# Kernel optimization log

Measured on AMD Instinct MI355X. Metric: run time of the kernel, lower is better.

Reference implementation:

```python
import jax, jax.numpy as jnp
import numpy as np
from functools import partial

L, B, D, V = 256, 64, 1024, 32000
N_LAYERS = 2  # wargs.enc_layer_cnt


def _ran_scan(x_seq, c0, Wix, Wic, Wfx, Wfc, Wcx, bi, bf, bc, reverse):
    """RAN over time. x_seq: [L,B,D], c0: [B,D]. Returns (h_seq [L,B,D], c_last).

    Cell: cand = x@Wcx + bc; i = sigma(x@Wix + c@Wic + bi); f = sigma(x@Wfx + c@Wfc + bf)
          c' = i*cand + f*c; h = tanh(c') + x  (residual=True)
    """
    # precompute input projections for all steps (hoisted out of the recurrence)
    xi = x_seq @ Wix + bi   # [L,B,D]
    xf = x_seq @ Wfx + bf
    xc = x_seq @ Wcx + bc

    def step(c, inputs):
        x, xi_t, xf_t, xc_t = inputs
        i = jax.nn.sigmoid(xi_t + c @ Wic)
        f = jax.nn.sigmoid(xf_t + c @ Wfc)
        c_new = i * xc_t + f * c
        h = jnp.tanh(c_new) + x
        return c_new, h

    c_last, hs = jax.lax.scan(step, c0, (x_seq, xi, xf, xc), reverse=reverse)
    return hs, c_last


def setup_inputs() -> dict:
    key = jax.random.key(0)
    ks = jax.random.split(key, 20)
    s = 1.0 / np.sqrt(D)
    xs = jax.random.randint(ks[0], (L, B), 0, V, dtype=jnp.int64)
    emb = jax.random.normal(ks[1], (V, D), dtype=jnp.float32) * s
    emb = emb.at[0].set(0.0)  # padding_idx=PAD(=0)
    def w(k):
        return jax.random.normal(k, (D, D), dtype=jnp.float32) * s
    inp = {"xs": xs, "emb": emb}
    for pfx, off in (("fw", 2), ("bw", 10)):
        inp[pfx + "_Wix"] = w(ks[off + 0])
        inp[pfx + "_Wic"] = w(ks[off + 1])
        inp[pfx + "_Wfx"] = w(ks[off + 2])
        inp[pfx + "_Wfc"] = w(ks[off + 3])
        inp[pfx + "_Wcx"] = w(ks[off + 4])
        inp[pfx + "_bi"] = jnp.zeros((D,), jnp.float32)
        inp[pfx + "_bf"] = jnp.zeros((D,), jnp.float32)
        inp[pfx + "_bc"] = jnp.zeros((D,), jnp.float32)
    return inp


def reference(xs, emb,
              fw_Wix, fw_Wic, fw_Wfx, fw_Wfc, fw_Wcx, fw_bi, fw_bf, fw_bc,
              bw_Wix, bw_Wic, bw_Wfx, bw_Wfc, bw_Wcx, bw_bi, bw_bf, bw_bc):
    x = emb[xs]                         # [L,B,D] token embeddings
    c = jnp.zeros((xs.shape[1], D), dtype=emb.dtype)  # c0 = zeros(B, output_size)
    for _ in range(N_LAYERS):
        # snaker: forward-direction RAN, state c threads into backward pass
        first, c = _ran_scan(x, c, fw_Wix, fw_Wic, fw_Wfx, fw_Wfc, fw_Wcx,
                             fw_bi, fw_bf, fw_bc, reverse=False)
        x, c = _ran_scan(first, c, bw_Wix, bw_Wic, bw_Wfx, bw_Wfc, bw_Wcx,
                         bw_bi, bw_bf, bw_bc, reverse=True)
    return x
```

## Files before the change

### kernel.cpp

```cpp
#include <hip/hip_runtime.h>
#include <hip/hip_bf16.h>

typedef unsigned int u32;
typedef unsigned short u16;
typedef unsigned long long u64;
typedef __attribute__((ext_vector_type(8))) short short8;
typedef __attribute__((ext_vector_type(4))) float floatx4;

#define L_SEQ 256
#define BATCH 64
#define DIM 1024
#define GROUPS 8
#define GWGS 32
#define GROWS 8

__device__ __forceinline__ float b2f(u16 u) {
  union { u32 i; float f; } v; v.i = ((u32)u) << 16; return v.f;
}
__device__ __forceinline__ u16 f2b(float f) {
  union { float f; u32 i; } v; v.f = f;
  u32 r = v.i + 0x7FFFu + ((v.i >> 16) & 1u);
  return (u16)(r >> 16);
}

__device__ __forceinline__ void st_b16_sc(const u16* p, u16 v) {
  asm volatile("global_store_short %0, %1, off sc0 sc1"
               :: "v"((u64)(uintptr_t)p), "v"((u32)v) : "memory");
}

__global__ void zero_cnt(u32* p) {
  #pragma unroll
  for (int i = 0; i < 4; ++i) p[threadIdx.x * 4 + i] = 0;
}

__global__ __launch_bounds__(256) void transpose6(
    const float* __restrict__ w0, const float* __restrict__ w1,
    const float* __restrict__ w2, const float* __restrict__ w3,
    const float* __restrict__ w4, const float* __restrict__ w5,
    u16* __restrict__ wt)
{
  __shared__ u16 tile[64][66];
  const int z = blockIdx.z;
  const float* src = z==0?w0: z==1?w1: z==2?w2: z==3?w3: z==4?w4: w5;
  u16* dst = wt + (size_t)z * DIM * DIM;
  const int k0 = blockIdx.x * 64, n0 = blockIdx.y * 64;
  const int r = threadIdx.x & 63, q = threadIdx.x >> 6;
  #pragma unroll 4
  for (int rep = 0; rep < 16; ++rep) {
    int k = q * 16 + rep;
    tile[k][r] = f2b(src[(size_t)(k0 + k) * DIM + n0 + r]);
  }
  __syncthreads();
  #pragma unroll 4
  for (int rep = 0; rep < 16; ++rep) {
    int n = q * 16 + rep;
    dst[(size_t)(n0 + n) * DIM + k0 + r] = tile[r][n];
  }
}

__global__ __launch_bounds__(256) void embed_gather(
    const int* __restrict__ xs, const float* __restrict__ emb, u16* __restrict__ Xb)
{
  const int t = blockIdx.x * 256 + threadIdx.x;
  const int row = t >> 8, ch = t & 255;
  const int tok = xs[row];
  float4 v = *(const float4*)(emb + (size_t)tok * DIM + ch * 4);
  union { ushort4 s; u16 u[4]; } o;
  o.u[0] = f2b(v.x); o.u[1] = f2b(v.y); o.u[2] = f2b(v.z); o.u[3] = f2b(v.w);
  *(ushort4*)(Xb + (size_t)row * DIM + ch * 4) = o.s;
}

__global__ __launch_bounds__(256) void proj3(
    const u16* __restrict__ X, const u16* __restrict__ WTbase,
    const float* __restrict__ bi, const float* __restrict__ bfp,
    const float* __restrict__ bc,
    u16* __restrict__ XI, u16* __restrict__ XF, u16* __restrict__ XC)
{
  __shared__ __align__(16) u16 ldsA[8 * 64 * 8];
  __shared__ __align__(16) u16 ldsB[8 * 64 * 8];
  const int z = blockIdx.z;
  const u16* WT = WTbase + (size_t)z * DIM * DIM;
  const float* bias = z == 0 ? bi : (z == 1 ? bfp : bc);
  u16* Y = z == 0 ? XI : (z == 1 ? XF : XC);
  const int m0 = blockIdx.x * 128, n0 = blockIdx.y * 128;
  const int tid = threadIdx.x;
  const int l = tid & 63, w = tid >> 6;
  const int wm = w >> 1, wn = w & 1;

  floatx4 acc[4][4];
  #pragma unroll
  for (int i = 0; i < 4; ++i)
    #pragma unroll
    for (int j = 0; j < 4; ++j) acc[i][j] = (floatx4){0, 0, 0, 0};

  const int srow = tid >> 2, sch = tid & 3;
  for (int k0 = 0; k0 < DIM; k0 += 32) {
    #pragma unroll
    for (int rr = 0; rr < 2; ++rr) {
      int row = rr * 64 + srow;
      uint4 va = *(const uint4*)(X  + (size_t)(m0 + row) * DIM + k0 + sch * 8);
      uint4 vb = *(const uint4*)(WT + (size_t)(n0 + row) * DIM + k0 + sch * 8);
      int slot = ((row >> 4) * 64 + (row & 15) + 16 * sch) * 8;
      *(uint4*)(ldsA + slot) = va;
      *(uint4*)(ldsB + slot) = vb;
    }
    __syncthreads();
    short8 af[4], bf8[4];
    #pragma unroll
    for (int i = 0; i < 4; ++i) af[i]  = *(const short8*)(ldsA + ((wm * 4 + i) * 64 + l) * 8);
    #pragma unroll
    for (int j = 0; j < 4; ++j) bf8[j] = *(const short8*)(ldsB + ((wn * 4 + j) * 64 + l) * 8);
    #pragma unroll
    for (int i = 0; i < 4; ++i)
      #pragma unroll
      for (int j = 0; j < 4; ++j)
        acc[i][j] = __builtin_amdgcn_mfma_f32_16x16x32_bf16(af[i], bf8[j], acc[i][j], 0, 0, 0);
    __syncthreads();
  }
  const int lq = l >> 4, lc = l & 15;
  #pragma unroll
  for (int j = 0; j < 4; ++j) {
    int col = n0 + wn * 64 + j * 16 + lc;
    float bv = bias[col];
    #pragma unroll
    for (int i = 0; i < 4; ++i)
      #pragma unroll
      for (int r = 0; r < 4; ++r) {
        int row = m0 + wm * 64 + i * 16 + lq * 4 + r;
        Y[(size_t)row * DIM + col] = f2b(acc[i][j][r] + bv);
      }
  }
}

__device__ __forceinline__ void g_arrive(u32* c) {
  __syncthreads();
  if (threadIdx.x == 0)
    __hip_atomic_fetch_add(c, 1u, __ATOMIC_RELAXED, __HIP_MEMORY_SCOPE_AGENT);
}
__device__ __forceinline__ void g_wait(u32* c, u32 tgt) {
  if (threadIdx.x == 0)
    while (__hip_atomic_load(c, __ATOMIC_RELAXED, __HIP_MEMORY_SCOPE_AGENT) < tgt)
      __builtin_amdgcn_s_sleep(1);
  __syncthreads();
}

__global__ __launch_bounds__(256, 1) void ran_scan_g(
    const float* __restrict__ Wic, const float* __restrict__ Wfc,
    const u16* __restrict__ XI, const u16* __restrict__ XF,
    const u16* __restrict__ XC,
    u16* __restrict__ Xb,
    float* __restrict__ HoutF,
    u16* __restrict__ cbf,
    float* __restrict__ cf32,
    u32* __restrict__ cnt,
    int reverse, int load_c, int write_out)
{
  __shared__ floatx4 part[4][2][2][64];
  const int tid = threadIdx.x, l = tid & 63, w = tid >> 6;
  const int group = blockIdx.x & 7, member = blockIdx.x >> 3;
  const int q = l >> 4, lr = l & 15;
  const int d0 = member * 32;
  const int g8 = group * GROWS;
  u16* cgrp = cbf + (size_t)group * (2 * GROWS * DIM);
  u32* gcnt = cnt + group * 32;
  const int act = (w == 0) && (q < 2);
  const int mrow = q * 4;

  short8 bregs[8][2][2];
  for (int kk8 = 0; kk8 < 8; ++kk8) {
    const int kbase = w * 256 + kk8 * 32 + q * 8;
    #pragma unroll
    for (int nt = 0; nt < 2; ++nt) {
      const int n = d0 + nt * 16 + lr;
      #pragma unroll
      for (int g = 0; g < 2; ++g) {
        const float* W = g ? Wfc : Wic;
        union { short8 v; u16 u[8]; } tmp;
        #pragma unroll
        for (int j = 0; j < 8; ++j) tmp.u[j] = f2b(W[(size_t)(kbase + j) * DIM + n]);
        bregs[kk8][nt][g] = tmp.v;
      }
    }
  }

  float creg[2][4];
  float xi[2][4], xf[2][4], xc[2][4], xv[2][4];
  int t = reverse ? (L_SEQ - 1) : 0;
  const int dt = reverse ? -1 : 1;

  if (act) {
    #pragma unroll
    for (int nt = 0; nt < 2; ++nt)
      #pragma unroll
      for (int r = 0; r < 4; ++r) {
        const int b = g8 + mrow + r, d = d0 + nt * 16 + lr;
        creg[nt][r] = load_c ? cf32[(size_t)b * DIM + d] : 0.0f;
        st_b16_sc(cgrp + (mrow + r) * DIM + d, f2b(creg[nt][r]));
      }
    const size_t base = (size_t)t * (BATCH * DIM);
    #pragma unroll
    for (int nt = 0; nt < 2; ++nt)
      #pragma unroll
      for (int r = 0; r < 4; ++r) {
        const size_t idx = base + (size_t)(g8 + mrow + r) * DIM + d0 + nt * 16 + lr;
        xi[nt][r] = b2f(XI[idx]); xf[nt][r] = b2f(XF[idx]);
        xc[nt][r] = b2f(XC[idx]); xv[nt][r] = b2f(Xb[idx]);
      }
  }

  u32 epoch = 1;
  g_arrive(gcnt);
  g_wait(gcnt, GWGS * epoch); ++epoch;

  for (int step = 0; step < L_SEQ; ++step, t += dt) {
    const size_t base = (size_t)t * (BATCH * DIM);
    const u16* crd = cgrp + (size_t)(step & 1) * (GROWS * DIM);
    u16* cwr = cgrp + (size_t)((step + 1) & 1) * (GROWS * DIM);

    uint4 afr[8];
    if (lr < 8) {
      const u64 ab = (u64)(uintptr_t)crd + (u32)(lr * 2048 + w * 512 + q * 16);
      asm volatile(
        "global_load_dwordx4 %0, %8, off sc0 sc1\n\t"
        "global_load_dwordx4 %1, %8, off offset:64 sc0 sc1\n\t"
        "global_load_dwordx4 %2, %8, off offset:128 sc0 sc1\n\t"
        "global_load_dwordx4 %3, %8, off offset:192 sc0 sc1\n\t"
        "global_load_dwordx4 %4, %8, off offset:256 sc0 sc1\n\t"
        "global_load_dwordx4 %5, %8, off offset:320 sc0 sc1\n\t"
        "global_load_dwordx4 %6, %8, off offset:384 sc0 sc1\n\t"
        "global_load_dwordx4 %7, %8, off offset:448 sc0 sc1\n\t"
        "s_waitcnt vmcnt(0)"
        : "=&v"(afr[0]), "=&v"(afr[1]), "=&v"(afr[2]), "=&v"(afr[3]),
          "=&v"(afr[4]), "=&v"(afr[5]), "=&v"(afr[6]), "=&v"(afr[7])
        : "v"(ab)
        : "memory");
    } else {
      #pragma unroll
      for (int i = 0; i < 8; ++i) afr[i] = (uint4){0, 0, 0, 0};
    }

    floatx4 acc[2][2];
    #pragma unroll
    for (int nt = 0; nt < 2; ++nt)
      #pragma unroll
      for (int g = 0; g < 2; ++g) acc[nt][g] = (floatx4){0, 0, 0, 0};
    #pragma unroll
    for (int kk8 = 0; kk8 < 8; ++kk8) {
      const short8 a = __builtin_bit_cast(short8, afr[kk8]);
      #pragma unroll
      for (int nt = 0; nt < 2; ++nt) {
        acc[nt][0] = __builtin_amdgcn_mfma_f32_16x16x32_bf16(a, bregs[kk8][nt][0], acc[nt][0], 0, 0, 0);
        acc[nt][1] = __builtin_amdgcn_mfma_f32_16x16x32_bf16(a, bregs[kk8][nt][1], acc[nt][1], 0, 0, 0);
      }
    }
    #pragma unroll
    for (int nt = 0; nt < 2; ++nt) {
      part[w][nt][0][l] = acc[nt][0];
      part[w][nt][1][l] = acc[nt][1];
    }
    __syncthreads();

    if (act) {
      floatx4 sI[2], sF[2];
      #pragma unroll
      for (int nt = 0; nt < 2; ++nt) {
        sI[nt] = part[0][nt][0][l]; sF[nt] = part[0][nt][1][l];
        #pragma unroll
        for (int pw = 1; pw < 4; ++pw) { sI[nt] += part[pw][nt][0][l]; sF[nt] += part[pw][nt][1][l]; }
      }
      #pragma unroll
      for (int nt = 0; nt < 2; ++nt)
        #pragma unroll
        for (int r = 0; r < 4; ++r) {
          const float iv = 1.0f / (1.0f + __expf(-(xi[nt][r] + sI[nt][r])));
          const float fv = 1.0f / (1.0f + __expf(-(xf[nt][r] + sF[nt][r])));
          const float cn = iv * xc[nt][r] + fv * creg[nt][r];
          creg[nt][r] = cn;
          const float hv = tanhf(cn) + xv[nt][r];
          const int d = d0 + nt * 16 + lr;
          const size_t idx = base + (size_t)(g8 + mrow + r) * DIM + d;
          __builtin_nontemporal_store(f2b(hv), Xb + idx);
          if (write_out) __builtin_nontemporal_store(hv, HoutF + idx);
          st_b16_sc(cwr + (mrow + r) * DIM + d, f2b(cn));
        }
    }
    g_arrive(gcnt);
    if (act && step + 1 < L_SEQ) {
      const size_t nb = (size_t)(t + dt) * (BATCH * DIM);
      #pragma unroll
      for (int nt = 0; nt < 2; ++nt)
        #pragma unroll
        for (int r = 0; r < 4; ++r) {
          const size_t idx = nb + (size_t)(g8 + mrow + r) * DIM + d0 + nt * 16 + lr;
          xi[nt][r] = b2f(XI[idx]); xf[nt][r] = b2f(XF[idx]);
          xc[nt][r] = b2f(XC[idx]); xv[nt][r] = b2f(Xb[idx]);
        }
    }
    g_wait(gcnt, GWGS * epoch); ++epoch;
  }

  if (act) {
    #pragma unroll
    for (int nt = 0; nt < 2; ++nt)
      #pragma unroll
      for (int r = 0; r < 4; ++r)
        cf32[(size_t)(g8 + mrow + r) * DIM + d0 + nt * 16 + lr] = creg[nt][r];
  }
}

extern "C" void kernel_launch(void* const* d_in, const int* in_sizes, int n_in,
                              void* d_out, int out_size, void* d_ws, size_t ws_size,
                              hipStream_t stream) {
  (void)in_sizes; (void)out_size; (void)ws_size;
  const int* xs = (const int*)d_in[0];
  const float* emb = (const float*)d_in[1];
  const float* W[18];
  for (int i = 0; i < 18 && i < n_in; ++i) W[i] = (const float*)d_in[i];

  char* ws = (char*)d_ws;
  u32* cnt    = (u32*)ws;
  u16* WT     = (u16*)(ws + 8192);
  u16* Xb     = (u16*)(ws + 12591104ull);
  u16* XIb    = (u16*)(ws + 46145536ull);
  u16* XFb    = (u16*)(ws + 79699968ull);
  u16* XCb    = (u16*)(ws + 113254400ull);
  u16* cbf    = (u16*)(ws + 146808832ull);
  float* cf32 = (float*)(ws + 147070976ull);

  zero_cnt<<<1, 256, 0, stream>>>(cnt);
  transpose6<<<dim3(16, 16, 6), 256, 0, stream>>>(W[2], W[4], W[6], W[10], W[12], W[14], WT);
  embed_gather<<<16384, 256, 0, stream>>>(xs, emb, Xb);

  for (int s = 0; s < 4; ++s) {
    const int p = s & 1;
    const u16* WTs = WT + (size_t)p * 3 * DIM * DIM;
    proj3<<<dim3(128, 8, 3), 256, 0, stream>>>(
        Xb, WTs, W[p ? 15 : 7], W[p ? 16 : 8], W[p ? 17 : 9], XIb, XFb, XCb);
    ran_scan_g<<<256, 256, 0, stream>>>(
        W[p ? 11 : 3], W[p ? 13 : 5], XIb, XFb, XCb, Xb, (float*)d_out,
        cbf, cf32, cnt + s * 256, p, s > 0 ? 1 : 0, s == 3 ? 1 : 0);
  }
}
```

Before: 4.701 ms.

## Use XCD-local atomic barrier and packed c-state publish in scan kernel

At startup each workgroup records its XCC id, and the kernel checks whether all 32 members of a group share one XCD. If they do, it takes a path that publishes the c state with non-coherent atomic swaps and polls the counter with atomics without sc1, avoiding device-wide cache coherence traffic. The c state is now written as packed dword stores in a permuted layout, and the weight k-index is remapped to match. The tanh and h output are moved after the publish, and input loads become nontemporal. The change adds a detection barrier, a bounded spin loop, and relies on the hardware placing each group on one XCD.

```diff
diff --git a/kernel.cpp b/kernel.cpp
--- a/kernel.cpp
+++ b/kernel.cpp
@@ -23,14 +23,87 @@
   return (u16)(r >> 16);
 }
 
-__device__ __forceinline__ void st_b16_sc(const u16* p, u16 v) {
-  asm volatile("global_store_short %0, %1, off sc0 sc1"
-               :: "v"((u64)(uintptr_t)p), "v"((u32)v) : "memory");
+__device__ __forceinline__ void st_u32_llc(u32* p, u32 v) {
+  asm volatile("global_store_dword %0, %1, off sc0 sc1"
+               :: "v"((u64)(uintptr_t)p), "v"(v) : "memory");
+}
+__device__ __forceinline__ u32 ld_u32_llc(const u32* p) {
+  u32 v;
+  asm volatile("global_load_dword %0, %1, off sc0 sc1\n\ts_waitcnt vmcnt(0)"
+               : "=v"(v) : "v"((u64)(uintptr_t)p) : "memory");
+  return v;
+}
+
+template<bool LOCAL>
+__device__ __forceinline__ void c_write_publish(
+    u32* gcnt, u16* cwr, int act, int cb_off,
+    u32 pk0, u32 pk1, u32 pk2, u32 pk3)
+{
+  if (act) {
+    const u64 a0 = (u64)(uintptr_t)cwr + (u32)cb_off;
+    const u64 a1 = a0 + 2048, a2 = a0 + 4096, a3 = a0 + 6144;
+    if constexpr (LOCAL) {
+      u32 o0, o1, o2, o3;
+      asm volatile(
+        "global_atomic_swap %0, %4, %8, off sc0\n\t"
+        "global_atomic_swap %1, %5, %9, off sc0\n\t"
+        "global_atomic_swap %2, %6, %10, off sc0\n\t"
+        "global_atomic_swap %3, %7, %11, off sc0\n\t"
+        "s_waitcnt vmcnt(0)"
+        : "=&v"(o0), "=&v"(o1), "=&v"(o2), "=&v"(o3)
+        : "v"(a0), "v"(a1), "v"(a2), "v"(a3),
+          "v"(pk0), "v"(pk1), "v"(pk2), "v"(pk3)
+        : "memory");
+    } else {
+      asm volatile(
+        "global_store_dword %0, %4, off sc0 sc1\n\t"
+        "global_store_dword %1, %5, off sc0 sc1\n\t"
+        "global_store_dword %2, %6, off sc0 sc1\n\t"
+        "global_store_dword %3, %7, off sc0 sc1\n\t"
+        "s_waitcnt vmcnt(0)"
+        :: "v"(a0), "v"(a1), "v"(a2), "v"(a3),
+           "v"(pk0), "v"(pk1), "v"(pk2), "v"(pk3)
+        : "memory");
+    }
+  }
+  __builtin_amdgcn_sched_barrier(0);
+  if (threadIdx.x == 0) {
+    if constexpr (LOCAL)
+      asm volatile("global_atomic_add %0, %1, off"
+                   :: "v"((u64)(uintptr_t)gcnt), "v"(1u) : "memory");
+    else
+      __hip_atomic_fetch_add(gcnt, 1u, __ATOMIC_RELAXED, __HIP_MEMORY_SCOPE_AGENT);
+  }
+}
+
+template<bool LOCAL>
+__device__ __forceinline__ void g_wait_t(u32* c, u32 tgt) {
+  if (threadIdx.x == 0) {
+    if constexpr (LOCAL) {
+      u32 v, it = 0;
+      const u64 a = (u64)(uintptr_t)c;
+      const u32 z = 0;
+      do {
+        asm volatile("global_atomic_add %0, %1, %2, off sc0\n\ts_waitcnt vmcnt(0)"
+                     : "=v"(v) : "v"(a), "v"(z) : "memory");
+      } while (v < tgt && ++it < (1u << 20));
+    } else {
+      while (__hip_atomic_load(c, __ATOMIC_RELAXED, __HIP_MEMORY_SCOPE_AGENT) < tgt)
+        __builtin_amdgcn_s_sleep(1);
+    }
+  }
+  __syncthreads();
+}
+
+__device__ __forceinline__ void g_arrive_full(u32* c) {
+  __syncthreads();
+  if (threadIdx.x == 0)
+    __hip_atomic_fetch_add(c, 1u, __ATOMIC_RELAXED, __HIP_MEMORY_SCOPE_AGENT);
 }
 
 __global__ void zero_cnt(u32* p) {
   #pragma unroll
-  for (int i = 0; i < 4; ++i) p[threadIdx.x * 4 + i] = 0;
+  for (int i = 0; i < 8; ++i) p[threadIdx.x * 8 + i] = 0;
 }
 
 __global__ __launch_bounds__(256) void transpose6(
@@ -132,56 +205,20 @@
   }
 }
 
-__device__ __forceinline__ void g_arrive(u32* c) {
-  __syncthreads();
-  if (threadIdx.x == 0)
-    __hip_atomic_fetch_add(c, 1u, __ATOMIC_RELAXED, __HIP_MEMORY_SCOPE_AGENT);
-}
-__device__ __forceinline__ void g_wait(u32* c, u32 tgt) {
-  if (threadIdx.x == 0)
-    while (__hip_atomic_load(c, __ATOMIC_RELAXED, __HIP_MEMORY_SCOPE_AGENT) < tgt)
-      __builtin_amdgcn_s_sleep(1);
-  __syncthreads();
-}
-
-__global__ __launch_bounds__(256, 1) void ran_scan_g(
-    const float* __restrict__ Wic, const float* __restrict__ Wfc,
+template<bool LOCAL>
+__device__ __forceinline__ void scan_body(
     const u16* __restrict__ XI, const u16* __restrict__ XF,
-    const u16* __restrict__ XC,
-    u16* __restrict__ Xb,
-    float* __restrict__ HoutF,
-    u16* __restrict__ cbf,
-    float* __restrict__ cf32,
-    u32* __restrict__ cnt,
-    int reverse, int load_c, int write_out)
-{
-  __shared__ floatx4 part[4][2][2][64];
+    const u16* __restrict__ XC, u16* __restrict__ Xb,
+    float* __restrict__ HoutF, u16* __restrict__ cgrp,
+    float* __restrict__ cf32, u32* gcnt,
+    const short8 (&bregs)[8][2][2], floatx4 (*part)[2][2][64],
+    int reverse, int load_c, int write_out, int g8, int d0)
+{
   const int tid = threadIdx.x, l = tid & 63, w = tid >> 6;
-  const int group = blockIdx.x & 7, member = blockIdx.x >> 3;
   const int q = l >> 4, lr = l & 15;
-  const int d0 = member * 32;
-  const int g8 = group * GROWS;
-  u16* cgrp = cbf + (size_t)group * (2 * GROWS * DIM);
-  u32* gcnt = cnt + group * 32;
   const int act = (w == 0) && (q < 2);
   const int mrow = q * 4;
-
-  short8 bregs[8][2][2];
-  for (int kk8 = 0; kk8 < 8; ++kk8) {
-    const int kbase = w * 256 + kk8 * 32 + q * 8;
-    #pragma unroll
-    for (int nt = 0; nt < 2; ++nt) {
-      const int n = d0 + nt * 16 + lr;
-      #pragma unroll
-      for (int g = 0; g < 2; ++g) {
-        const float* W = g ? Wfc : Wic;
-        union { short8 v; u16 u[8]; } tmp;
-        #pragma unroll
-        for (int j = 0; j < 8; ++j) tmp.u[j] = f2b(W[(size_t)(kbase + j) * DIM + n]);
-        bregs[kk8][nt][g] = tmp.v;
-      }
-    }
-  }
+  const int cb_off = mrow * 2048 + 2 * d0 + 4 * lr;
 
   float creg[2][4];
   float xi[2][4], xf[2][4], xc[2][4], xv[2][4];
@@ -195,22 +232,34 @@
       for (int r = 0; r < 4; ++r) {
         const int b = g8 + mrow + r, d = d0 + nt * 16 + lr;
         creg[nt][r] = load_c ? cf32[(size_t)b * DIM + d] : 0.0f;
-        st_b16_sc(cgrp + (mrow + r) * DIM + d, f2b(creg[nt][r]));
-      }
+      }
+  }
+  {
+    u32 pk0 = 0, pk1 = 0, pk2 = 0, pk3 = 0;
+    if (act) {
+      pk0 = (u32)f2b(creg[0][0]) | ((u32)f2b(creg[1][0]) << 16);
+      pk1 = (u32)f2b(creg[0][1]) | ((u32)f2b(creg[1][1]) << 16);
+      pk2 = (u32)f2b(creg[0][2]) | ((u32)f2b(creg[1][2]) << 16);
+      pk3 = (u32)f2b(creg[0][3]) | ((u32)f2b(creg[1][3]) << 16);
+    }
+    c_write_publish<LOCAL>(gcnt, cgrp, act, cb_off, pk0, pk1, pk2, pk3);
+  }
+  if (act) {
     const size_t base = (size_t)t * (BATCH * DIM);
     #pragma unroll
     for (int nt = 0; nt < 2; ++nt)
       #pragma unroll
       for (int r = 0; r < 4; ++r) {
         const size_t idx = base + (size_t)(g8 + mrow + r) * DIM + d0 + nt * 16 + lr;
-        xi[nt][r] = b2f(XI[idx]); xf[nt][r] = b2f(XF[idx]);
-        xc[nt][r] = b2f(XC[idx]); xv[nt][r] = b2f(Xb[idx]);
+        xi[nt][r] = b2f(__builtin_nontemporal_load(XI + idx));
+        xf[nt][r] = b2f(__builtin_nontemporal_load(XF + idx));
+        xc[nt][r] = b2f(__builtin_nontemporal_load(XC + idx));
+        xv[nt][r] = b2f(__builtin_nontemporal_load(Xb + idx));
       }
   }
 
   u32 epoch = 1;
-  g_arrive(gcnt);
-  g_wait(gcnt, GWGS * epoch); ++epoch;
+  g_wait_t<LOCAL>(gcnt, GWGS * epoch); ++epoch;
 
   for (int step = 0; step < L_SEQ; ++step, t += dt) {
     const size_t base = (size_t)t * (BATCH * DIM);
@@ -274,29 +323,46 @@
         for (int r = 0; r < 4; ++r) {
           const float iv = 1.0f / (1.0f + __expf(-(xi[nt][r] + sI[nt][r])));
           const float fv = 1.0f / (1.0f + __expf(-(xf[nt][r] + sF[nt][r])));
-          const float cn = iv * xc[nt][r] + fv * creg[nt][r];
-          creg[nt][r] = cn;
-          const float hv = tanhf(cn) + xv[nt][r];
+          creg[nt][r] = iv * xc[nt][r] + fv * creg[nt][r];
+        }
+    }
+    {
+      u32 pk0 = 0, pk1 = 0, pk2 = 0, pk3 = 0;
+      if (act) {
+        pk0 = (u32)f2b(creg[0][0]) | ((u32)f2b(creg[1][0]) << 16);
+        pk1 = (u32)f2b(creg[0][1]) | ((u32)f2b(creg[1][1]) << 16);
+        pk2 = (u32)f2b(creg[0][2]) | ((u32)f2b(creg[1][2]) << 16);
+        pk3 = (u32)f2b(creg[0][3]) | ((u32)f2b(creg[1][3]) << 16);
+      }
+      c_write_publish<LOCAL>(gcnt, cwr, act, cb_off, pk0, pk1, pk2, pk3);
+    }
+
+    if (act) {
+      #pragma unroll
+      for (int nt = 0; nt < 2; ++nt)
+        #pragma unroll
+        for (int r = 0; r < 4; ++r) {
+          const float hv = tanhf(creg[nt][r]) + xv[nt][r];
           const int d = d0 + nt * 16 + lr;
           const size_t idx = base + (size_t)(g8 + mrow + r) * DIM + d;
           __builtin_nontemporal_store(f2b(hv), Xb + idx);
           if (write_out) __builtin_nontemporal_store(hv, HoutF + idx);
-          st_b16_sc(cwr + (mrow + r) * DIM + d, f2b(cn));
         }
-    }
-    g_arrive(gcnt);
-    if (act && step + 1 < L_SEQ) {
-      const size_t nb = (size_t)(t + dt) * (BATCH * DIM);
-      #pragma unroll
-      for (int nt = 0; nt < 2; ++nt)
+      if (step + 1 < L_SEQ) {
+        const size_t nb = (size_t)(t + dt) * (BATCH * DIM);
         #pragma unroll
-        for (int r = 0; r < 4; ++r) {
-          const size_t idx = nb + (size_t)(g8 + mrow + r) * DIM + d0 + nt * 16 + lr;
-          xi[nt][r] = b2f(XI[idx]); xf[nt][r] = b2f(XF[idx]);
-          xc[nt][r] = b2f(XC[idx]); xv[nt][r] = b2f(Xb[idx]);
-        }
-    }
-    g_wait(gcnt, GWGS * epoch); ++epoch;
+        for (int nt = 0; nt < 2; ++nt)
+          #pragma unroll
+          for (int r = 0; r < 4; ++r) {
+            const size_t idx = nb + (size_t)(g8 + mrow + r) * DIM + d0 + nt * 16 + lr;
+            xi[nt][r] = b2f(__builtin_nontemporal_load(XI + idx));
+            xf[nt][r] = b2f(__builtin_nontemporal_load(XF + idx));
+            xc[nt][r] = b2f(__builtin_nontemporal_load(XC + idx));
+            xv[nt][r] = b2f(__builtin_nontemporal_load(Xb + idx));
+          }
+      }
+    }
+    g_wait_t<LOCAL>(gcnt, GWGS * epoch); ++epoch;
   }
 
   if (act) {
@@ -306,6 +372,67 @@
       for (int r = 0; r < 4; ++r)
         cf32[(size_t)(g8 + mrow + r) * DIM + d0 + nt * 16 + lr] = creg[nt][r];
   }
+}
+
+__global__ __launch_bounds__(256, 1) void ran_scan_g(
+    const float* __restrict__ Wic, const float* __restrict__ Wfc,
+    const u16* __restrict__ XI, const u16* __restrict__ XF,
+    const u16* __restrict__ XC,
+    u16* __restrict__ Xb,
+    float* __restrict__ HoutF,
+    u16* __restrict__ cbf,
+    float* __restrict__ cf32,
+    u32* __restrict__ cnt,
+    u32* __restrict__ fcnt,
+    u32* __restrict__ xcdtab,
+    int reverse, int load_c, int write_out)
+{
+  __shared__ floatx4 part[4][2][2][64];
+  const int tid = threadIdx.x, l = tid & 63, w = tid >> 6;
+  const int group = blockIdx.x & 7, member = blockIdx.x >> 3;
+  const int q = l >> 4, lr = l & 15;
+  const int d0 = member * 32;
+  const int g8 = group * GROWS;
+  u16* cgrp = cbf + (size_t)group * (2 * GROWS * DIM);
+
+  short8 bregs[8][2][2];
+  for (int kk8 = 0; kk8 < 8; ++kk8) {
+    const int kbase = w * 256 + kk8 * 32 + q * 8;
+    #pragma unroll
+    for (int nt = 0; nt < 2; ++nt) {
+      const int n = d0 + nt * 16 + lr;
+      #pragma unroll
+      for (int g = 0; g < 2; ++g) {
+        const float* W = g ? Wfc : Wic;
+        union { short8 v; u16 u[8]; } tmp;
+        #pragma unroll
+        for (int j = 0; j < 8; ++j) {
+          const int k = kbase + j;
+          const int p = k & 31;
+          const int orig = (k & ~31) | ((p & 1) << 4) | (p >> 1);
+          tmp.u[j] = f2b(W[(size_t)orig * DIM + n]);
+        }
+        bregs[kk8][nt][g] = tmp.v;
+      }
+    }
+  }
+
+  u32 xcc;
+  asm volatile("s_getreg_b32 %0, hwreg(HW_REG_XCC_ID)" : "=s"(xcc));
+  u32* gchk = cnt + group * 32 + 8;
+  if (tid == 0) st_u32_llc(xcdtab + group * 32 + member, xcc);
+  g_arrive_full(gchk);
+  g_wait_t<false>(gchk, GWGS);
+  u32 o = xcc;
+  if (l < 32) o = ld_u32_llc(xcdtab + group * 32 + l);
+  const int lok = __all(o == xcc);
+
+  if (lok)
+    scan_body<true>(XI, XF, XC, Xb, HoutF, cgrp, cf32, fcnt + group * 16,
+                    bregs, part, reverse, load_c, write_out, g8, d0);
+  else
+    scan_body<false>(XI, XF, XC, Xb, HoutF, cgrp, cf32, cnt + group * 32,
+                     bregs, part, reverse, load_c, write_out, g8, d0);
 }
 
 extern "C" void kernel_launch(void* const* d_in, const int* in_sizes, int n_in,
@@ -338,6 +465,7 @@
         Xb, WTs, W[p ? 15 : 7], W[p ? 16 : 8], W[p ? 17 : 9], XIb, XFb, XCb);
     ran_scan_g<<<256, 256, 0, stream>>>(
         W[p ? 11 : 3], W[p ? 13 : 5], XIb, XFb, XCb, Xb, (float*)d_out,
-        cbf, cf32, cnt + s * 256, p, s > 0 ? 1 : 0, s == 3 ? 1 : 0);
-  }
-}
+        cbf, cf32, cnt + s * 256, cnt + 1024 + s * 128, cnt + 1536,
+        p, s > 0 ? 1 : 0, s == 3 ? 1 : 0);
+  }
+}
```

Result: slower. 4.797 ms (+2.0%).
